# Kernel tuning notes

Hardware: AMD Instinct MI355X
Metric: run time of the kernel (lower is better)

The kernel has to match this reference:

```python
import jax, jax.numpy as jnp
import numpy as np

D_MODEL = 768
NUM_HEADS = 12
D_K = D_MODEL // NUM_HEADS


def setup_inputs() -> dict:
    key = jax.random.key(0)
    ks = jax.random.split(key, 9)
    B, S = 2, 4096
    x = jax.random.normal(ks[0], (B, S, D_MODEL), dtype=jnp.float32)
    s = 1.0 / np.sqrt(D_MODEL)
    Wq = jax.random.normal(ks[1], (D_MODEL, D_MODEL), dtype=jnp.float32) * s
    Wk = jax.random.normal(ks[2], (D_MODEL, D_MODEL), dtype=jnp.float32) * s
    Wv = jax.random.normal(ks[3], (D_MODEL, D_MODEL), dtype=jnp.float32) * s
    Wo = jax.random.normal(ks[4], (D_MODEL, D_MODEL), dtype=jnp.float32) * s
    bq = jnp.zeros((D_MODEL,), dtype=jnp.float32)
    bk = jnp.zeros((D_MODEL,), dtype=jnp.float32)
    bv = jnp.zeros((D_MODEL,), dtype=jnp.float32)
    bo = jnp.zeros((D_MODEL,), dtype=jnp.float32)
    return {"x": x, "Wq": Wq, "bq": bq, "Wk": Wk, "bk": bk,
            "Wv": Wv, "bv": bv, "Wo": Wo, "bo": bo}


def _split_heads(t):
    B, S, _ = t.shape
    return t.reshape(B, S, NUM_HEADS, D_K).transpose(0, 2, 1, 3)  # [B,H,S,d_k]


def reference(x, Wq, bq, Wk, bk, Wv, bv, Wo, bo):
    Q = _split_heads(x @ Wq.T + bq)
    K = _split_heads(x @ Wk.T + bk)
    V = _split_heads(x @ Wv.T + bv)
    scale = 1.0 / jnp.sqrt(jnp.float32(D_K))
    scores = jnp.einsum('bhqd,bhkd->bhqk', Q, K) * scale  # [B,H,S,S]
    attn = jax.nn.softmax(scores, axis=-1)
    out = jnp.einsum('bhqk,bhkd->bhqd', attn, V)          # [B,H,S,d_k]
    B, _, S, _ = out.shape
    out = out.transpose(0, 2, 1, 3).reshape(B, S, D_MODEL)
    return out @ Wo.T + bo
```

## Files before the change

kernel.cpp:

```cpp
#include <hip/hip_runtime.h>
#include <hip/hip_bf16.h>
#include <stdint.h>

typedef __hip_bfloat16 bf16;
typedef __attribute__((ext_vector_type(8))) short short8;
typedef __attribute__((ext_vector_type(4))) float f32x4;
typedef __attribute__((ext_vector_type(16))) float f32x16;

#define MFMA16(a, b, c) __builtin_amdgcn_mfma_f32_16x16x32_bf16((a), (b), (c), 0, 0, 0)
#define MFMA32(a, b, c) __builtin_amdgcn_mfma_f32_32x32x16_bf16((a), (b), (c), 0, 0, 0)

__device__ __forceinline__ unsigned short f2bf(float f) {
  bf16 h = __float2bfloat16(f);
  unsigned short u;
  __builtin_memcpy(&u, &h, 2);
  return u;
}

__device__ __forceinline__ float bf2f(unsigned short u) {
  uint32_t x = ((uint32_t)u) << 16;
  float f;
  __builtin_memcpy(&f, &x, 4);
  return f;
}

__device__ __forceinline__ uint32_t cvtpk(float lo, float hi) {
  uint32_t r;
  asm("v_cvt_pk_bf16_f32 %0, %1, %2" : "=v"(r) : "v"(lo), "v"(hi));
  return r;
}

__device__ __forceinline__ void pl32swap(uint32_t& a, uint32_t& b) {
  asm volatile("v_permlane32_swap_b32 %0, %1" : "+v"(a), "+v"(b));
}

__device__ __forceinline__ void gload_lds16(const void* g, void* l) {
  __builtin_amdgcn_global_load_lds(
      (const __attribute__((address_space(1))) uint32_t*)g,
      (__attribute__((address_space(3))) uint32_t*)l, 16, 0, 0);
}

__device__ __forceinline__ int swz_chunk(int row, int c) { return c ^ (row & 7); }

__global__ __launch_bounds__(256) void cvt_all(
    const float* __restrict__ x,
    const float* __restrict__ w0, const float* __restrict__ w1,
    const float* __restrict__ w2, const float* __restrict__ w3,
    bf16* __restrict__ xo,
    bf16* __restrict__ o0, bf16* __restrict__ o1,
    bf16* __restrict__ o2, bf16* __restrict__ o3) {
  int idx = blockIdx.x * 256 + threadIdx.x;
  const float* src;
  bf16* dst;
  int i;
  if (idx < 1572864) {
    src = x; dst = xo; i = idx;
  } else {
    int r = idx - 1572864;
    int w = r / 147456;
    i = r - w * 147456;
    src = (w == 0) ? w0 : (w == 1) ? w1 : (w == 2) ? w2 : w3;
    dst = (w == 0) ? o0 : (w == 1) ? o1 : (w == 2) ? o2 : o3;
  }
  float4 v = ((const float4*)src)[i];
  ushort4 u;
  u.x = f2bf(v.x); u.y = f2bf(v.y); u.z = f2bf(v.z); u.w = f2bf(v.w);
  ((ushort4*)dst)[i] = u;
}

__global__ __launch_bounds__(256, 4) void gemm_qkv(
    const bf16* __restrict__ A,
    const bf16* __restrict__ Wqb, const bf16* __restrict__ Wkb,
    const bf16* __restrict__ Wvb,
    const float* __restrict__ bq, const float* __restrict__ bk,
    const float* __restrict__ bv,
    bf16* __restrict__ Qh, bf16* __restrict__ Kh, bf16* __restrict__ Vtt,
    float sq) {
  __shared__ bf16 As[128 * 64];
  __shared__ bf16 Bs[128 * 64];
  const int tid = threadIdx.x;
  const int lane = tid & 63, wid = tid >> 6;
  const int wr = wid >> 1, wc = wid & 1;
  const int l15 = lane & 15, lhi = lane >> 4;
  const int tm = blockIdx.x * 128;
  const int by = blockIdx.y;
  const int seg = by / 6;
  const int tn = (by - seg * 6) * 128;

  const bf16* B = (seg == 0) ? Wqb : (seg == 1) ? Wkb : Wvb;
  const float* bias = (seg == 0) ? bq : (seg == 1) ? bk : bv;
  const float scale = (seg == 0) ? sq : 1.0f;
  const int K = 768;

  f32x4 zero = {0.f, 0.f, 0.f, 0.f};
  f32x4 acc[4][4];
  for (int i = 0; i < 4; ++i)
    for (int j = 0; j < 4; ++j) acc[i][j] = zero;

  for (int k0 = 0; k0 < K; k0 += 64) {
    __syncthreads();
    for (int it = 0; it < 4; ++it) {
      int o = (tid + it * 256) << 4;
      int row = o >> 7, c = (o >> 4) & 7;
      int sw = swz_chunk(row, c) << 4;
      gload_lds16((const char*)A + (((size_t)(tm + row) * K + k0) << 1) + sw, (char*)As + o);
      gload_lds16((const char*)B + (((size_t)(tn + row) * K + k0) << 1) + sw, (char*)Bs + o);
    }
    __syncthreads();
    for (int ks = 0; ks < 2; ++ks) {
      short8 af[4], bfr[4];
      for (int mi = 0; mi < 4; ++mi) {
        int row = wr * 64 + mi * 16 + l15;
        af[mi] = *(const short8*)((const char*)As + row * 128 +
                                  (swz_chunk(row, ks * 4 + lhi) << 4));
      }
      for (int ni = 0; ni < 4; ++ni) {
        int row = wc * 64 + ni * 16 + l15;
        bfr[ni] = *(const short8*)((const char*)Bs + row * 128 +
                                   (swz_chunk(row, ks * 4 + lhi) << 4));
      }
      for (int mi = 0; mi < 4; ++mi)
        for (int ni = 0; ni < 4; ++ni)
          acc[mi][ni] = MFMA16(af[mi], bfr[ni], acc[mi][ni]);
    }
  }

  if (seg == 2) {
    for (int mi = 0; mi < 4; ++mi)
      for (int ni = 0; ni < 4; ++ni) {
        int m0 = tm + wr * 64 + mi * 16 + lhi * 4;
        int n = tn + wc * 64 + ni * 16 + l15;
        int b = m0 >> 12, s = m0 & 4095, hh = n >> 6, d = n & 63;
        float bia = bias[n];
        ushort4 us;
        us.x = f2bf(acc[mi][ni][0] + bia);
        us.y = f2bf(acc[mi][ni][1] + bia);
        us.z = f2bf(acc[mi][ni][2] + bia);
        us.w = f2bf(acc[mi][ni][3] + bia);
        size_t e = (size_t)(b * 12 + hh) * 262144 + (size_t)(s >> 6) * 4096 +
                   (size_t)((s >> 3) & 7) * 512 + d * 8 + (s & 7);
        *(ushort4*)(Vtt + e) = us;
      }
  } else {
    bf16* dst = (seg == 0) ? Qh : Kh;
    for (int mi = 0; mi < 4; ++mi)
      for (int ni = 0; ni < 4; ++ni)
        for (int j = 0; j < 4; ++j) {
          int m = tm + wr * 64 + mi * 16 + lhi * 4 + j;
          int n = tn + wc * 64 + ni * 16 + l15;
          float v = (acc[mi][ni][j] + bias[n]) * scale;
          int b = m >> 12, s = m & 4095, hh = n >> 6, d = n & 63;
          dst[(((size_t)(b * 12 + hh) * 4096 + s) << 6) + d] = __float2bfloat16(v);
        }
  }
}

__global__ __launch_bounds__(256, 4) void gemm_wo(
    const bf16* __restrict__ A, const bf16* __restrict__ B,
    const float* __restrict__ bias, float* __restrict__ C) {
  __shared__ bf16 As[128 * 64];
  __shared__ bf16 Bs[64 * 64];
  const int tid = threadIdx.x;
  const int lane = tid & 63, wid = tid >> 6;
  const int l15 = lane & 15, lhi = lane >> 4;
  const int tm = blockIdx.x * 128, tn = blockIdx.y * 64;
  const int K = 768;

  f32x4 zero = {0.f, 0.f, 0.f, 0.f};
  f32x4 acc[2][4];
  for (int i = 0; i < 2; ++i)
    for (int j = 0; j < 4; ++j) acc[i][j] = zero;

  for (int k0 = 0; k0 < K; k0 += 64) {
    __syncthreads();
    for (int it = 0; it < 4; ++it) {
      int o = (tid + it * 256) << 4;
      int row = o >> 7, c = (o >> 4) & 7;
      int sw = swz_chunk(row, c) << 4;
      gload_lds16((const char*)A + (((size_t)(tm + row) * K + k0) << 1) + sw, (char*)As + o);
    }
    for (int it = 0; it < 2; ++it) {
      int o = (tid + it * 256) << 4;
      int row = o >> 7, c = (o >> 4) & 7;
      int sw = swz_chunk(row, c) << 4;
      gload_lds16((const char*)B + (((size_t)(tn + row) * K + k0) << 1) + sw, (char*)Bs + o);
    }
    __syncthreads();
    for (int ks = 0; ks < 2; ++ks) {
      short8 af[2], bfr[4];
      for (int mi = 0; mi < 2; ++mi) {
        int row = wid * 32 + mi * 16 + l15;
        af[mi] = *(const short8*)((const char*)As + row * 128 +
                                  (swz_chunk(row, ks * 4 + lhi) << 4));
      }
      for (int ni = 0; ni < 4; ++ni) {
        int row = ni * 16 + l15;
        bfr[ni] = *(const short8*)((const char*)Bs + row * 128 +
                                   (swz_chunk(row, ks * 4 + lhi) << 4));
      }
      for (int mi = 0; mi < 2; ++mi)
        for (int ni = 0; ni < 4; ++ni)
          acc[mi][ni] = MFMA16(af[mi], bfr[ni], acc[mi][ni]);
    }
  }

  for (int mi = 0; mi < 2; ++mi)
    for (int ni = 0; ni < 4; ++ni)
      for (int j = 0; j < 4; ++j) {
        int m = tm + wid * 32 + mi * 16 + lhi * 4 + j;
        int n = tn + ni * 16 + l15;
        C[(size_t)m * 768 + n] = acc[mi][ni][j] + bias[n];
      }
}

template <int SPLIT>
__global__ __launch_bounds__(256, 3) void attn_kernel(
    const bf16* __restrict__ Qh, const bf16* __restrict__ Kh,
    const bf16* __restrict__ VTT, bf16* __restrict__ AO,
    bf16* __restrict__ OP0, bf16* __restrict__ OP1,
    float* __restrict__ PS0, float* __restrict__ PS1) {
  __shared__ float4 smem4[34816 / 16];
  char* smraw = (char*)smem4;
#define KT(b) (smraw + (b) * 8192)
#define VT(b) (smraw + 16384 + (b) * 8192)
  float* OX = (float*)smraw;

  const int tid = threadIdx.x;
  const int lane = tid & 63, wid = tid >> 6;
  const int l31 = lane & 31, h = lane >> 5;
  const int qsub = wid & 1, kvh = wid >> 1;

  const int i = blockIdx.x;
  const int xcd = i & 7, slot = i >> 3;
  int bh, qt, kvp;
  if (SPLIT) {
    bh = xcd * 3 + (slot >> 6);
    int r = slot & 63;
    qt = r >> 1;
    kvp = r & 1;
  } else {
    bh = xcd * 3 + (slot >> 5);
    qt = slot & 31;
    kvp = 0;
  }
  const int NT = SPLIT ? 32 : 64;
  const int kv0 = kvp * 32;

  const size_t hb = (size_t)bh * 262144;
  const bf16* Qb = Qh + hb;
  const bf16* Kb = Kh + hb;
  const char* Vbc = (const char*)(VTT + hb);
  const int qb = qt * 128 + qsub * 64;

  short8 qf[2][4];
#pragma unroll
  for (int j = 0; j < 2; ++j)
#pragma unroll
    for (int ki = 0; ki < 4; ++ki)
      qf[j][ki] = *(const short8*)((const char*)Qb + (size_t)(qb + 32 * j + l31) * 128 +
                                   ki * 32 + h * 16);

  f32x16 z16;
  for (int i2 = 0; i2 < 16; ++i2) z16[i2] = 0.f;
  f32x16 o00 = z16, o01 = z16, o10 = z16, o11 = z16;
  float psum0 = 0.f, psum1 = 0.f;

  const int krow = kvh * 32 + l31;

  for (int it = 0; it < 2; ++it) {
    int o = (tid + it * 256) << 4;
    int row = o >> 7, c = (o >> 4) & 7;
    gload_lds16((const char*)Kb + (size_t)kv0 * 8192 + row * 128 +
                    (swz_chunk(row, c) << 4), KT(0) + o);
    gload_lds16(Vbc + (size_t)kv0 * 8192 + (swz_chunk(row, c) << 10) + (row << 4),
                VT(0) + o);
  }
  __syncthreads();

  int cur = 0;
  for (int kt = 0; kt < NT; ++kt) {
    if (kt < NT - 1) {
      const size_t akt = (size_t)(kv0 + kt + 1);
      const char* Kg = (const char*)Kb + akt * 8192;
      const char* Vg = Vbc + akt * 8192;
      char* Kd = KT(cur ^ 1);
      char* Vd = VT(cur ^ 1);
      for (int it = 0; it < 2; ++it) {
        int o = (tid + it * 256) << 4;
        int row = o >> 7, c = (o >> 4) & 7;
        gload_lds16(Kg + row * 128 + (swz_chunk(row, c) << 4), Kd + o);
        gload_lds16(Vg + (swz_chunk(row, c) << 10) + (row << 4), Vd + o);
      }
    }

    const char* Kl = KT(cur);
    const char* Vl = VT(cur);

    f32x16 s0, s1;
    __builtin_amdgcn_s_setprio(1);
    {
      short8 kf = *(const short8*)(Kl + krow * 128 + (swz_chunk(krow, h) << 4));
      s0 = MFMA32(kf, qf[0][0], z16);
      s1 = MFMA32(kf, qf[1][0], z16);
    }
#pragma unroll
    for (int ki = 1; ki < 4; ++ki) {
      short8 kf = *(const short8*)(Kl + krow * 128 + (swz_chunk(krow, 2 * ki + h) << 4));
      s0 = MFMA32(kf, qf[0][ki], s0);
      s1 = MFMA32(kf, qf[1][ki], s1);
    }
    __builtin_amdgcn_s_setprio(0);

    short8 pb[2][2];
#pragma unroll
    for (int j = 0; j < 2; ++j) {
#pragma unroll
      for (int kk = 0; kk < 2; ++kk) {
        float p[8];
#pragma unroll
        for (int e = 0; e < 8; ++e)
          p[e] = __builtin_amdgcn_exp2f(j ? s1[8 * kk + e] : s0[8 * kk + e]);
        float ps = ((p[0] + p[1]) + (p[2] + p[3])) + ((p[4] + p[5]) + (p[6] + p[7]));
        if (j) psum1 += ps; else psum0 += ps;
        uint32_t A0 = cvtpk(p[0], p[1]), A1 = cvtpk(p[2], p[3]);
        uint32_t B0 = cvtpk(p[4], p[5]), B1 = cvtpk(p[6], p[7]);
        pl32swap(A0, B0);
        pl32swap(A1, B1);
        uint32_t w[4] = {A0, A1, B0, B1};
        short8 frag;
        __builtin_memcpy(&frag, w, 16);
        pb[j][kk] = frag;
      }
    }

    __builtin_amdgcn_s_setprio(1);
#pragma unroll
    for (int kk = 0; kk < 2; ++kk) {
      short8 v0 = *(const short8*)(Vl + l31 * 128 +
                                   (swz_chunk(l31, 4 * kvh + 2 * kk + h) << 4));
      short8 v1 = *(const short8*)(Vl + (32 + l31) * 128 +
                                   (swz_chunk(32 + l31, 4 * kvh + 2 * kk + h) << 4));
      o00 = MFMA32(v0, pb[0][kk], o00);
      o01 = MFMA32(v0, pb[1][kk], o01);
      o10 = MFMA32(v1, pb[0][kk], o10);
      o11 = MFMA32(v1, pb[1][kk], o11);
    }
    __builtin_amdgcn_s_setprio(0);

    __syncthreads();
    cur ^= 1;
  }

  psum0 += __shfl_xor(psum0, 32);
  psum1 += __shfl_xor(psum1, 32);

  float* W = OX + (size_t)(qsub * 64 + lane) * 68;
  if (kvh == 1) {
#pragma unroll
    for (int g = 0; g < 4; ++g) {
      *(float4*)(W + 0 * 16 + 4 * g) = make_float4(o00[4*g], o00[4*g+1], o00[4*g+2], o00[4*g+3]);
      *(float4*)(W + 1 * 16 + 4 * g) = make_float4(o01[4*g], o01[4*g+1], o01[4*g+2], o01[4*g+3]);
      *(float4*)(W + 2 * 16 + 4 * g) = make_float4(o10[4*g], o10[4*g+1], o10[4*g+2], o10[4*g+3]);
      *(float4*)(W + 3 * 16 + 4 * g) = make_float4(o11[4*g], o11[4*g+1], o11[4*g+2], o11[4*g+3]);
    }
    W[64] = psum0;
    W[65] = psum1;
  }
  __syncthreads();
  if (kvh == 0) {
#pragma unroll
    for (int g = 0; g < 4; ++g) {
      float4 a0 = *(const float4*)(W + 0 * 16 + 4 * g);
      float4 a1 = *(const float4*)(W + 1 * 16 + 4 * g);
      float4 a2 = *(const float4*)(W + 2 * 16 + 4 * g);
      float4 a3 = *(const float4*)(W + 3 * 16 + 4 * g);
      o00[4*g] += a0.x; o00[4*g+1] += a0.y; o00[4*g+2] += a0.z; o00[4*g+3] += a0.w;
      o01[4*g] += a1.x; o01[4*g+1] += a1.y; o01[4*g+2] += a1.z; o01[4*g+3] += a1.w;
      o10[4*g] += a2.x; o10[4*g+1] += a2.y; o10[4*g+2] += a2.z; o10[4*g+3] += a2.w;
      o11[4*g] += a3.x; o11[4*g+1] += a3.y; o11[4*g+2] += a3.z; o11[4*g+3] += a3.w;
    }
    psum0 += W[64];
    psum1 += W[65];

    const int b = bh / 12, hd = bh % 12;
    if (SPLIT) {
      bf16* OPp = kvp ? OP1 : OP0;
      float* PSp = kvp ? PS1 : PS0;
#pragma unroll
      for (int j = 0; j < 2; ++j) {
        int q = qb + 32 * j + l31;
        char* base = (char*)OPp + (((size_t)(b * 4096 + q)) * 768 + hd * 64) * 2;
#pragma unroll
        for (int t = 0; t < 2; ++t) {
#pragma unroll
          for (int u = 0; u < 4; ++u) {
            ushort4 us;
            float v0 = (t ? (j ? o11[4*u+0] : o10[4*u+0]) : (j ? o01[4*u+0] : o00[4*u+0]));
            float v1 = (t ? (j ? o11[4*u+1] : o10[4*u+1]) : (j ? o01[4*u+1] : o00[4*u+1]));
            float v2 = (t ? (j ? o11[4*u+2] : o10[4*u+2]) : (j ? o01[4*u+2] : o00[4*u+2]));
            float v3 = (t ? (j ? o11[4*u+3] : o10[4*u+3]) : (j ? o01[4*u+3] : o00[4*u+3]));
            us.x = f2bf(v0); us.y = f2bf(v1); us.z = f2bf(v2); us.w = f2bf(v3);
            int d0 = 32 * t + 8 * u + 4 * h;
            *(ushort4*)(base + d0 * 2) = us;
          }
        }
        PSp[(size_t)bh * 4096 + q] = j ? psum1 : psum0;
      }
    } else {
      float pinv0 = 1.0f / psum0;
      float pinv1 = 1.0f / psum1;
#pragma unroll
      for (int j = 0; j < 2; ++j) {
        int q = qb + 32 * j + l31;
        char* base = (char*)AO + (((size_t)(b * 4096 + q)) * 768 + hd * 64) * 2;
        float pv = j ? pinv1 : pinv0;
#pragma unroll
        for (int t = 0; t < 2; ++t) {
#pragma unroll
          for (int u = 0; u < 4; ++u) {
            ushort4 us;
            float v0 = (t ? (j ? o11[4*u+0] : o10[4*u+0]) : (j ? o01[4*u+0] : o00[4*u+0]));
            float v1 = (t ? (j ? o11[4*u+1] : o10[4*u+1]) : (j ? o01[4*u+1] : o00[4*u+1]));
            float v2 = (t ? (j ? o11[4*u+2] : o10[4*u+2]) : (j ? o01[4*u+2] : o00[4*u+2]));
            float v3 = (t ? (j ? o11[4*u+3] : o10[4*u+3]) : (j ? o01[4*u+3] : o00[4*u+3]));
            us.x = f2bf(v0 * pv); us.y = f2bf(v1 * pv);
            us.z = f2bf(v2 * pv); us.w = f2bf(v3 * pv);
            int d0 = 32 * t + 8 * u + 4 * h;
            *(ushort4*)(base + d0 * 2) = us;
          }
        }
      }
    }
  }
#undef KT
#undef VT
}

__global__ __launch_bounds__(256) void combine_kernel(
    const bf16* __restrict__ OP0, const bf16* __restrict__ OP1,
    const float* __restrict__ PS0, const float* __restrict__ PS1,
    bf16* __restrict__ AO) {
  int t = blockIdx.x * 256 + threadIdx.x;
  size_t e0 = (size_t)t * 8;
  int row = (int)(e0 / 768);
  int col = (int)(e0 - (size_t)row * 768);
  int hd = col >> 6;
  int bh = (row >> 12) * 12 + hd;
  int q = row & 4095;
  float r = 1.0f / (PS0[(size_t)bh * 4096 + q] + PS1[(size_t)bh * 4096 + q]);
  ushort4 a0 = *(const ushort4*)(OP0 + e0);
  ushort4 a1 = *(const ushort4*)(OP0 + e0 + 4);
  ushort4 b0 = *(const ushort4*)(OP1 + e0);
  ushort4 b1 = *(const ushort4*)(OP1 + e0 + 4);
  ushort4 o0, o1;
  o0.x = f2bf((bf2f(a0.x) + bf2f(b0.x)) * r);
  o0.y = f2bf((bf2f(a0.y) + bf2f(b0.y)) * r);
  o0.z = f2bf((bf2f(a0.z) + bf2f(b0.z)) * r);
  o0.w = f2bf((bf2f(a0.w) + bf2f(b0.w)) * r);
  o1.x = f2bf((bf2f(a1.x) + bf2f(b1.x)) * r);
  o1.y = f2bf((bf2f(a1.y) + bf2f(b1.y)) * r);
  o1.z = f2bf((bf2f(a1.z) + bf2f(b1.z)) * r);
  o1.w = f2bf((bf2f(a1.w) + bf2f(b1.w)) * r);
  *(ushort4*)(AO + e0) = o0;
  *(ushort4*)(AO + e0 + 4) = o1;
}

extern "C" void kernel_launch(void* const* d_in, const int* in_sizes, int n_in,
                              void* d_out, int out_size, void* d_ws, size_t ws_size,
                              hipStream_t stream) {
  (void)in_sizes; (void)n_in; (void)out_size;
  const float* x  = (const float*)d_in[0];
  const float* Wq = (const float*)d_in[1];
  const float* bq = (const float*)d_in[2];
  const float* Wk = (const float*)d_in[3];
  const float* bk = (const float*)d_in[4];
  const float* Wv = (const float*)d_in[5];
  const float* bv = (const float*)d_in[6];
  const float* Wo = (const float*)d_in[7];
  const float* bo = (const float*)d_in[8];

  char* ws = (char*)d_ws;
  bf16* Qh  = (bf16*)(ws + 0);
  bf16* Kh  = (bf16*)(ws + 12582912);
  bf16* VTT = (bf16*)(ws + 25165824);
  bf16* xb  = (bf16*)(ws + 37748736);
  bf16* Wqb = (bf16*)(ws + 50331648);
  bf16* Wkb = (bf16*)(ws + 51511296);
  bf16* Wvb = (bf16*)(ws + 52690944);
  bf16* Wob = (bf16*)(ws + 53870592);
  bf16* OP0 = xb;
  bf16* OP1 = (bf16*)(ws + 55050240);
  float* PS0 = (float*)(ws + 67633152);
  float* PS1 = (float*)(ws + 68026368);
  const size_t NEED = 68419584;

  cvt_all<<<8448, 256, 0, stream>>>(x, Wq, Wk, Wv, Wo, xb, Wqb, Wkb, Wvb, Wob);

  const float SQ = 0.125f * 1.4426950408889634f;
  dim3 gq(64, 18);
  gemm_qkv<<<gq, 256, 0, stream>>>(xb, Wqb, Wkb, Wvb, bq, bk, bv,
                                   Qh, Kh, VTT, SQ);
  dim3 gw(64, 12);
  if (ws_size >= NEED) {
    attn_kernel<1><<<1536, 256, 0, stream>>>(Qh, Kh, VTT, nullptr,
                                             OP0, OP1, PS0, PS1);
    bf16* AOq = Qh;
    combine_kernel<<<3072, 256, 0, stream>>>(OP0, OP1, PS0, PS1, AOq);
    gemm_wo<<<gw, 256, 0, stream>>>(AOq, Wob, bo, (float*)d_out);
  } else {
    bf16* AO = xb;
    attn_kernel<0><<<768, 256, 0, stream>>>(Qh, Kh, VTT, AO,
                                            nullptr, nullptr, nullptr, nullptr);
    gemm_wo<<<gw, 256, 0, stream>>>(AO, Wob, bo, (float*)d_out);
  }
}
```

Before: 188.3 us.

## Quad-buffer K/V tiles and process two tiles per barrier in attention

```diff
diff --git a/kernel.cpp b/kernel.cpp
--- a/kernel.cpp
+++ b/kernel.cpp
@@ -214,15 +214,15 @@
 }
 
 template <int SPLIT>
-__global__ __launch_bounds__(256, 3) void attn_kernel(
+__global__ __launch_bounds__(256, 2) void attn_kernel(
     const bf16* __restrict__ Qh, const bf16* __restrict__ Kh,
     const bf16* __restrict__ VTT, bf16* __restrict__ AO,
     bf16* __restrict__ OP0, bf16* __restrict__ OP1,
     float* __restrict__ PS0, float* __restrict__ PS1) {
-  __shared__ float4 smem4[34816 / 16];
+  __shared__ float4 smem4[65536 / 16];
   char* smraw = (char*)smem4;
-#define KT(b) (smraw + (b) * 8192)
-#define VT(b) (smraw + 16384 + (b) * 8192)
+#define KB4(b) (smraw + (b) * 8192)
+#define VB4(b) (smraw + 32768 + (b) * 8192)
   float* OX = (float*)smraw;
 
   const int tid = threadIdx.x;
@@ -267,89 +267,87 @@
 
   const int krow = kvh * 32 + l31;
 
-  for (int it = 0; it < 2; ++it) {
-    int o = (tid + it * 256) << 4;
-    int row = o >> 7, c = (o >> 4) & 7;
-    gload_lds16((const char*)Kb + (size_t)kv0 * 8192 + row * 128 +
-                    (swz_chunk(row, c) << 4), KT(0) + o);
-    gload_lds16(Vbc + (size_t)kv0 * 8192 + (swz_chunk(row, c) << 10) + (row << 4),
-                VT(0) + o);
-  }
+#define STAGE(akt, b)                                                      \
+  for (int it = 0; it < 2; ++it) {                                         \
+    int o = (tid + it * 256) << 4;                                         \
+    int row = o >> 7, c = (o >> 4) & 7;                                    \
+    gload_lds16((const char*)Kb + (size_t)(akt) * 8192 + row * 128 +       \
+                    (swz_chunk(row, c) << 4), KB4(b) + o);                 \
+    gload_lds16(Vbc + (size_t)(akt) * 8192 + (swz_chunk(row, c) << 10) +   \
+                    (row << 4), VB4(b) + o);                               \
+  }
+
+#define PROCESS(b)                                                         \
+  {                                                                        \
+    const char* Kl = KB4(b);                                               \
+    const char* Vl = VB4(b);                                               \
+    f32x16 s0, s1;                                                         \
+    __builtin_amdgcn_s_setprio(1);                                         \
+    {                                                                      \
+      short8 kf = *(const short8*)(Kl + krow * 128 + (swz_chunk(krow, h) << 4)); \
+      s0 = MFMA32(kf, qf[0][0], z16);                                      \
+      s1 = MFMA32(kf, qf[1][0], z16);                                      \
+    }                                                                      \
+    _Pragma("unroll")                                                      \
+    for (int ki = 1; ki < 4; ++ki) {                                       \
+      short8 kf = *(const short8*)(Kl + krow * 128 +                       \
+                                   (swz_chunk(krow, 2 * ki + h) << 4));    \
+      s0 = MFMA32(kf, qf[0][ki], s0);                                      \
+      s1 = MFMA32(kf, qf[1][ki], s1);                                      \
+    }                                                                      \
+    __builtin_amdgcn_s_setprio(0);                                         \
+    short8 pb[2][2];                                                       \
+    _Pragma("unroll")                                                      \
+    for (int j = 0; j < 2; ++j) {                                          \
+      _Pragma("unroll")                                                    \
+      for (int kk = 0; kk < 2; ++kk) {                                     \
+        float p[8];                                                        \
+        _Pragma("unroll")                                                  \
+        for (int e = 0; e < 8; ++e)                                        \
+          p[e] = __builtin_amdgcn_exp2f(j ? s1[8 * kk + e] : s0[8 * kk + e]); \
+        float ps = ((p[0] + p[1]) + (p[2] + p[3])) + ((p[4] + p[5]) + (p[6] + p[7])); \
+        if (j) psum1 += ps; else psum0 += ps;                              \
+        uint32_t A0 = cvtpk(p[0], p[1]), A1 = cvtpk(p[2], p[3]);           \
+        uint32_t B0 = cvtpk(p[4], p[5]), B1 = cvtpk(p[6], p[7]);           \
+        pl32swap(A0, B0);                                                  \
+        pl32swap(A1, B1);                                                  \
+        uint32_t w_[4] = {A0, A1, B0, B1};                                 \
+        short8 frag;                                                       \
+        __builtin_memcpy(&frag, w_, 16);                                   \
+        pb[j][kk] = frag;                                                  \
+      }                                                                    \
+    }                                                                      \
+    __builtin_amdgcn_s_setprio(1);                                         \
+    _Pragma("unroll")                                                      \
+    for (int kk = 0; kk < 2; ++kk) {                                       \
+      short8 v0 = *(const short8*)(Vl + l31 * 128 +                        \
+                                   (swz_chunk(l31, 4 * kvh + 2 * kk + h) << 4)); \
+      short8 v1 = *(const short8*)(Vl + (32 + l31) * 128 +                 \
+                                   (swz_chunk(32 + l31, 4 * kvh + 2 * kk + h) << 4)); \
+      o00 = MFMA32(v0, pb[0][kk], o00);                                    \
+      o01 = MFMA32(v0, pb[1][kk], o01);                                    \
+      o10 = MFMA32(v1, pb[0][kk], o10);                                    \
+      o11 = MFMA32(v1, pb[1][kk], o11);                                    \
+    }                                                                      \
+    __builtin_amdgcn_s_setprio(0);                                         \
+  }
+
+  STAGE(kv0 + 0, 0);
+  STAGE(kv0 + 1, 1);
   __syncthreads();
 
-  int cur = 0;
-  for (int kt = 0; kt < NT; ++kt) {
-    if (kt < NT - 1) {
-      const size_t akt = (size_t)(kv0 + kt + 1);
-      const char* Kg = (const char*)Kb + akt * 8192;
-      const char* Vg = Vbc + akt * 8192;
-      char* Kd = KT(cur ^ 1);
-      char* Vd = VT(cur ^ 1);
-      for (int it = 0; it < 2; ++it) {
-        int o = (tid + it * 256) << 4;
-        int row = o >> 7, c = (o >> 4) & 7;
-        gload_lds16(Kg + row * 128 + (swz_chunk(row, c) << 4), Kd + o);
-        gload_lds16(Vg + (swz_chunk(row, c) << 10) + (row << 4), Vd + o);
-      }
-    }
-
-    const char* Kl = KT(cur);
-    const char* Vl = VT(cur);
-
-    f32x16 s0, s1;
-    __builtin_amdgcn_s_setprio(1);
-    {
-      short8 kf = *(const short8*)(Kl + krow * 128 + (swz_chunk(krow, h) << 4));
-      s0 = MFMA32(kf, qf[0][0], z16);
-      s1 = MFMA32(kf, qf[1][0], z16);
-    }
-#pragma unroll
-    for (int ki = 1; ki < 4; ++ki) {
-      short8 kf = *(const short8*)(Kl + krow * 128 + (swz_chunk(krow, 2 * ki + h) << 4));
-      s0 = MFMA32(kf, qf[0][ki], s0);
-      s1 = MFMA32(kf, qf[1][ki], s1);
-    }
-    __builtin_amdgcn_s_setprio(0);
-
-    short8 pb[2][2];
-#pragma unroll
-    for (int j = 0; j < 2; ++j) {
-#pragma unroll
-      for (int kk = 0; kk < 2; ++kk) {
-        float p[8];
-#pragma unroll
-        for (int e = 0; e < 8; ++e)
-          p[e] = __builtin_amdgcn_exp2f(j ? s1[8 * kk + e] : s0[8 * kk + e]);
-        float ps = ((p[0] + p[1]) + (p[2] + p[3])) + ((p[4] + p[5]) + (p[6] + p[7]));
-        if (j) psum1 += ps; else psum0 += ps;
-        uint32_t A0 = cvtpk(p[0], p[1]), A1 = cvtpk(p[2], p[3]);
-        uint32_t B0 = cvtpk(p[4], p[5]), B1 = cvtpk(p[6], p[7]);
-        pl32swap(A0, B0);
-        pl32swap(A1, B1);
-        uint32_t w[4] = {A0, A1, B0, B1};
-        short8 frag;
-        __builtin_memcpy(&frag, w, 16);
-        pb[j][kk] = frag;
-      }
-    }
-
-    __builtin_amdgcn_s_setprio(1);
-#pragma unroll
-    for (int kk = 0; kk < 2; ++kk) {
-      short8 v0 = *(const short8*)(Vl + l31 * 128 +
-                                   (swz_chunk(l31, 4 * kvh + 2 * kk + h) << 4));
-      short8 v1 = *(const short8*)(Vl + (32 + l31) * 128 +
-                                   (swz_chunk(32 + l31, 4 * kvh + 2 * kk + h) << 4));
-      o00 = MFMA32(v0, pb[0][kk], o00);
-      o01 = MFMA32(v0, pb[1][kk], o01);
-      o10 = MFMA32(v1, pb[0][kk], o10);
-      o11 = MFMA32(v1, pb[1][kk], o11);
-    }
-    __builtin_amdgcn_s_setprio(0);
-
+  for (int r = 0; r < NT / 2; ++r) {
+    int t0 = 2 * r;
+    if (r < NT / 2 - 1) {
+      STAGE(kv0 + t0 + 2, (t0 + 2) & 3);
+      STAGE(kv0 + t0 + 3, (t0 + 3) & 3);
+    }
+    PROCESS(t0 & 3);
+    PROCESS((t0 + 1) & 3);
     __syncthreads();
-    cur ^= 1;
-  }
+  }
+#undef STAGE
+#undef PROCESS
 
   psum0 += __shfl_xor(psum0, 32);
   psum1 += __shfl_xor(psum1, 32);
@@ -432,8 +430,8 @@
       }
     }
   }
-#undef KT
-#undef VT
+#undef KB4
+#undef VB4
 }
 
 __global__ __launch_bounds__(256) void combine_kernel(
```

After: 194.1 us. +3.1%, slower.
